# Optimization experiments

Hardware: AMD Instinct MI355X
Metric: run time of the kernel (lower is better)

## Reference

```python
import jax, jax.numpy as jnp
import numpy as np

N, E, H, G = 50000, 600000, 128, 512
PI = 3.141592653589793
EPS = 1e-5
NEG_SLOPE = 0.2


def _p(key, shape, scale):
    return jax.random.normal(key, shape, dtype=jnp.float32) * scale


def setup_inputs() -> dict:
    key = jax.random.key(0)
    ks = jax.random.split(key, 32)
    s = 1.0 / np.sqrt(H)
    inp = {
        "x": jax.random.normal(ks[0], (N, H), dtype=jnp.float32),
        "edge_index": jax.random.randint(ks[1], (2, E), 0, N, dtype=jnp.int32),
        "edge_attr": jax.random.normal(ks[2], (E, H), dtype=jnp.float32),
        "batch": jnp.sort(jax.random.randint(ks[3], (N,), 0, G, dtype=jnp.int32)),
    }
    # GATv2Conv layer 1 params
    inp.update(Wl1=_p(ks[4], (H, H), s), bl1=jnp.zeros((H,)), Wr1=_p(ks[5], (H, H), s), br1=jnp.zeros((H,)),
               We1=_p(ks[6], (H, H), s), att1=_p(ks[7], (H,), s), cb1=jnp.zeros((H,)))
    # GATv2Conv layer 2 params
    inp.update(Wl2=_p(ks[8], (H, H), s), bl2=jnp.zeros((H,)), Wr2=_p(ks[9], (H, H), s), br2=jnp.zeros((H,)),
               We2=_p(ks[10], (H, H), s), att2=_p(ks[11], (H,), s), cb2=jnp.zeros((H,)))
    # BatchNorm params
    inp.update(g1=jnp.ones((H,)), be1=jnp.zeros((H,)), g2=jnp.ones((H,)), be2=jnp.zeros((H,)))
    # AttentionalAggregation gate MLP (AggregationModuleTanh)
    inp.update(A1=_p(ks[12], (H, H), s), a1=jnp.zeros((H,)), A2=_p(ks[13], (H, H), s), a2=jnp.zeros((H,)))
    # final Linear
    inp.update(Wf=_p(ks[14], (H, H), s), bf=jnp.zeros((H,)))
    return inp


def gatv2(x, src, dst, eattr, Wl, bl, Wr, br, We, att, cb):
    n = x.shape[0]
    # add self loops, edge_attr fill_value='mean' (PyG default): per-dst mean of edge_attr
    deg = jax.ops.segment_sum(jnp.ones_like(dst, dtype=x.dtype), dst, num_segments=n)
    loop_attr = jax.ops.segment_sum(eattr, dst, num_segments=n) / jnp.maximum(deg, 1.0)[:, None]
    ar = jnp.arange(n, dtype=src.dtype)
    src2 = jnp.concatenate([src, ar])
    dst2 = jnp.concatenate([dst, ar])
    ea2 = jnp.concatenate([eattr, loop_attr], axis=0)
    xl = x @ Wl + bl  # source transform
    xr = x @ Wr + br  # target transform
    m = xl[src2] + xr[dst2] + ea2 @ We  # [E+N, H]
    m = jnp.where(m > 0, m, NEG_SLOPE * m)  # leaky_relu(0.2)
    e = m @ att  # [E+N]
    emax = jax.ops.segment_max(e, dst2, num_segments=n)
    ex = jnp.exp(e - emax[dst2])
    den = jax.ops.segment_sum(ex, dst2, num_segments=n)
    alpha = ex / den[dst2]
    out = jax.ops.segment_sum(alpha[:, None] * xl[src2], dst2, num_segments=n)
    return out + cb


def batchnorm(x, g, b):
    mu = jnp.mean(x, axis=0)
    var = jnp.var(x, axis=0)
    return (x - mu) * jax.lax.rsqrt(var + EPS) * g + b


def attn_pool(x, batch, A1, a1, A2, a2, n_graphs):
    gate = jnp.tanh(x @ A1 + a1) @ A2 + a2  # [N, H]
    gmax = jax.ops.segment_max(gate, batch, num_segments=n_graphs)
    ex = jnp.exp(gate - gmax[batch])
    den = jax.ops.segment_sum(ex, batch, num_segments=n_graphs)
    alpha = ex / jnp.maximum(den, 1e-16)[batch]
    return jax.ops.segment_sum(alpha * x, batch, num_segments=n_graphs)


def reference(x, edge_index, edge_attr, batch,
              Wl1, bl1, Wr1, br1, We1, att1, cb1,
              Wl2, bl2, Wr2, br2, We2, att2, cb2,
              g1, be1, g2, be2, A1, a1, A2, a2, Wf, bf):
    src, dst = edge_index[0], edge_index[1]
    h = gatv2(x, src, dst, edge_attr, Wl1, bl1, Wr1, br1, We1, att1, cb1)
    h = jnp.tanh(batchnorm(h, g1, be1))  # dropout = identity (eval)
    h = gatv2(h, src, dst, edge_attr, Wl2, bl2, Wr2, br2, We2, att2, cb2)
    h = jnp.tanh(batchnorm(h, g2, be2))
    pooled = attn_pool(h, batch, A1, a1, A2, a2, G)  # [G, H]
    out = jnp.tanh(pooled @ Wf + bf)
    axis = out * PI
    aperture = jnp.zeros_like(axis)
    return axis, aperture
```

## Files before the change

kernel.cpp:

```cpp
#include <hip/hip_runtime.h>
#include <hip/hip_bf16.h>
#include <math.h>

constexpr int NN = 50000;
constexpr int NE = 600000;
constexpr int HD = 128;
constexpr int NG = 512;
constexpr float EPSV = 1e-5f;
constexpr float PI_F = 3.14159265358979323846f;

static __device__ __forceinline__ float wave_reduce(float v) {
#pragma unroll
  for (int off = 32; off > 0; off >>= 1) v += __shfl_xor(v, off, 64);
  return v;
}

__global__ void deg_hist(const int* __restrict__ dst, int* __restrict__ deg) {
  int i = blockIdx.x * 256 + threadIdx.x;
  if (i < NE) atomicAdd(&deg[dst[i]], 1);
}

__global__ void scanA(const int* __restrict__ deg, int* __restrict__ part) {
  __shared__ int sh[256];
  int b = blockIdx.x, tid = threadIdx.x;
  int sum = 0;
  for (int k = tid; k < 1024; k += 256) {
    int idx = b * 1024 + k;
    if (idx < NN) sum += deg[idx];
  }
  sh[tid] = sum; __syncthreads();
  for (int s = 128; s; s >>= 1) { if (tid < s) sh[tid] += sh[tid + s]; __syncthreads(); }
  if (tid == 0) part[b] = sh[0];
}

__global__ void scanB(int* __restrict__ part, int nb) {
  if (threadIdx.x == 0) {
    int run = 0;
    for (int i = 0; i < nb; ++i) { int v = part[i]; part[i] = run; run += v; }
  }
}

__global__ void scanC(const int* __restrict__ deg, const int* __restrict__ part,
                      int* __restrict__ rowstart, int* __restrict__ cursor) {
  __shared__ int sh[256];
  int b = blockIdx.x, tid = threadIdx.x;
  int base = b * 1024 + tid * 4;
  int v[4];
#pragma unroll
  for (int k = 0; k < 4; ++k) v[k] = (base + k < NN) ? deg[base + k] : 0;
  int tot = v[0] + v[1] + v[2] + v[3];
  sh[tid] = tot; __syncthreads();
  for (int off = 1; off < 256; off <<= 1) {
    int x = (tid >= off) ? sh[tid - off] : 0;
    __syncthreads();
    sh[tid] += x;
    __syncthreads();
  }
  int excl = part[b] + sh[tid] - tot;
#pragma unroll
  for (int k = 0; k < 4; ++k) {
    if (base + k < NN) { rowstart[base + k] = excl; cursor[base + k] = excl; excl += v[k]; }
  }
}

__global__ void scatter_k(const int* __restrict__ src, const int* __restrict__ dst,
                          int* __restrict__ cursor, int* __restrict__ ceid, int* __restrict__ csrc) {
  int i = blockIdx.x * 256 + threadIdx.x;
  if (i < NE) {
    int d = dst[i];
    int pos = atomicAdd(&cursor[d], 1);
    ceid[pos] = i;
    csrc[pos] = src[i];
  }
}

__global__ void sloop_k(const float* __restrict__ eattr, const int* __restrict__ rowstart,
                        const int* __restrict__ deg, const int* __restrict__ ceid,
                        float* __restrict__ sloop) {
  int tid = threadIdx.x;
  int j = tid & 127, half = tid >> 7;
  int n = blockIdx.x * 2 + half;
  if (n >= NN) return;
  int st = rowstart[n], cnt = deg[n];
  float a = 0.f;
  for (int k = 0; k < cnt; ++k) {
    int e = ceid[st + k];
    a += eattr[(size_t)e * HD + j];
  }
  sloop[(size_t)n * HD + j] = a / (float)max(cnt, 1);
}

template <int DUAL, int ACT>
__global__ __launch_bounds__(256) void node_gemm(
    const float* __restrict__ in, const float* __restrict__ W1, const float* __restrict__ b1,
    const float* __restrict__ W2, const float* __restrict__ b2,
    float* __restrict__ o1, float* __restrict__ o2) {
  __shared__ float xs[32][HD];
  const int tid = threadIdx.x;
  const int j = tid & 127;
  const int half = tid >> 7;
  const int r0 = blockIdx.x * 32;
  for (int k = tid; k < 32 * HD / 4; k += 256) {
    int r = k >> 5, c4 = k & 31;
    float4 v = make_float4(0.f, 0.f, 0.f, 0.f);
    if (r0 + r < NN) v = ((const float4*)(in + (size_t)(r0 + r) * HD))[c4];
    *((float4*)&xs[r][c4 * 4]) = v;
  }
  __syncthreads();
  float acc1[16], acc2[16];
  const float bb1 = b1[j];
#pragma unroll
  for (int k = 0; k < 16; ++k) acc1[k] = bb1;
  if (DUAL) {
    const float bb2 = b2[j];
#pragma unroll
    for (int k = 0; k < 16; ++k) acc2[k] = bb2;
  }
#pragma unroll 4
  for (int i = 0; i < HD; i += 4) {
    const float w10 = W1[(i + 0) * HD + j], w11 = W1[(i + 1) * HD + j];
    const float w12 = W1[(i + 2) * HD + j], w13 = W1[(i + 3) * HD + j];
    float w20 = 0.f, w21 = 0.f, w22 = 0.f, w23 = 0.f;
    if (DUAL) {
      w20 = W2[(i + 0) * HD + j]; w21 = W2[(i + 1) * HD + j];
      w22 = W2[(i + 2) * HD + j]; w23 = W2[(i + 3) * HD + j];
    }
#pragma unroll
    for (int k = 0; k < 16; ++k) {
      const float4 a = *(const float4*)&xs[half * 16 + k][i];
      acc1[k] = fmaf(a.x, w10, fmaf(a.y, w11, fmaf(a.z, w12, fmaf(a.w, w13, acc1[k]))));
      if (DUAL)
        acc2[k] = fmaf(a.x, w20, fmaf(a.y, w21, fmaf(a.z, w22, fmaf(a.w, w23, acc2[k]))));
    }
  }
#pragma unroll
  for (int k = 0; k < 16; ++k) {
    int r = r0 + half * 16 + k;
    if (r < NN) {
      float v1 = acc1[k];
      if (ACT) v1 = tanhf(v1);
      o1[(size_t)r * HD + j] = v1;
      if (DUAL) o2[(size_t)r * HD + j] = acc2[k];
    }
  }
}

constexpr int ETOT = NE + NN;
constexpr int NTIL = (ETOT + 63) / 64;

static __device__ __forceinline__ void stage_ea(const float* __restrict__ eattr,
                                                const float* __restrict__ sloop,
                                                float* buf, int e0, int w, int lane) {
#pragma unroll
  for (int t = 0; t < 4; ++t) {
    const int rr = (w * 4 + t) * 2 + (lane >> 5);
    const int e = e0 + rr;
    const float* gp;
    if (e < NE) gp = eattr + (size_t)e * HD + (lane & 31) * 4;
    else if (e < ETOT) gp = sloop + (size_t)(e - NE) * HD + (lane & 31) * 4;
    else gp = eattr + (lane & 31) * 4;
    __builtin_amdgcn_global_load_lds(
        (const __attribute__((address_space(1))) void*)gp,
        (__attribute__((address_space(3))) void*)(buf + (w * 4 + t) * 256),
        16, 0, 0);
  }
}

__global__ __launch_bounds__(512, 2) void edge_scores(
    const float* __restrict__ eattr, const float* __restrict__ sloop,
    const int* __restrict__ src, const int* __restrict__ dst,
    const float* __restrict__ xl, const float* __restrict__ xr,
    const float* __restrict__ We, const float* __restrict__ att,
    float* __restrict__ ev) {
  __shared__ float We_s[HD * HD];
  __shared__ float ea_s[2][64 * HD];
  const int tid = threadIdx.x;
  const int tc = tid & 31;
  const int teg = tid >> 5;
  const int w = tid >> 6;
  const int lane = tid & 63;

  for (int k = tid; k < HD * HD / 4; k += 512)
    ((float4*)We_s)[k] = ((const float4*)We)[k];
  const float4 attv = ((const float4*)att)[tc];

  int it = blockIdx.x;
  int cur = 0;
  if (it < NTIL) stage_ea(eattr, sloop, ea_s[0], it * 64, w, lane);

  for (; it < NTIL; it += gridDim.x) {
    asm volatile("s_waitcnt vmcnt(0)" ::: "memory");
    __syncthreads();
    const int nxt = it + (int)gridDim.x;
    if (nxt < NTIL) stage_ea(eattr, sloop, ea_s[cur ^ 1], nxt * 64, w, lane);

    const float* ea = ea_s[cur];
    float acc[4][4];
#pragma unroll
    for (int m = 0; m < 4; ++m)
#pragma unroll
      for (int c = 0; c < 4; ++c) acc[m][c] = 0.f;

#pragma unroll 4
    for (int k0 = 0; k0 < HD; k0 += 4) {
      const float4 w0 = *(const float4*)&We_s[(k0 + 0) * HD + tc * 4];
      const float4 w1 = *(const float4*)&We_s[(k0 + 1) * HD + tc * 4];
      const float4 w2 = *(const float4*)&We_s[(k0 + 2) * HD + tc * 4];
      const float4 w3 = *(const float4*)&We_s[(k0 + 3) * HD + tc * 4];
#pragma unroll
      for (int m = 0; m < 4; ++m) {
        const float4 a = *(const float4*)&ea[(teg * 4 + m) * HD + k0];
        acc[m][0] = fmaf(a.x, w0.x, fmaf(a.y, w1.x, fmaf(a.z, w2.x, fmaf(a.w, w3.x, acc[m][0]))));
        acc[m][1] = fmaf(a.x, w0.y, fmaf(a.y, w1.y, fmaf(a.z, w2.y, fmaf(a.w, w3.y, acc[m][1]))));
        acc[m][2] = fmaf(a.x, w0.z, fmaf(a.y, w1.z, fmaf(a.z, w2.z, fmaf(a.w, w3.z, acc[m][2]))));
        acc[m][3] = fmaf(a.x, w0.w, fmaf(a.y, w1.w, fmaf(a.z, w2.w, fmaf(a.w, w3.w, acc[m][3]))));
      }
    }

    const int e0 = it * 64;
#pragma unroll
    for (int m = 0; m < 4; ++m) {
      const int e = e0 + teg * 4 + m;
      const bool valid = e < ETOT;
      int s_, d_;
      if (e < NE) { s_ = src[e]; d_ = dst[e]; }
      else if (valid) { s_ = d_ = e - NE; }
      else { s_ = d_ = 0; }
      const float4 xa = ((const float4*)(xl + (size_t)s_ * HD))[tc];
      const float4 xb = ((const float4*)(xr + (size_t)d_ * HD))[tc];
      float v0 = acc[m][0] + xa.x + xb.x; v0 = v0 > 0.f ? v0 : 0.2f * v0;
      float v1 = acc[m][1] + xa.y + xb.y; v1 = v1 > 0.f ? v1 : 0.2f * v1;
      float v2 = acc[m][2] + xa.z + xb.z; v2 = v2 > 0.f ? v2 : 0.2f * v2;
      float v3 = acc[m][3] + xa.w + xb.w; v3 = v3 > 0.f ? v3 : 0.2f * v3;
      float p = fmaf(v0, attv.x, fmaf(v1, attv.y, fmaf(v2, attv.z, v3 * attv.w)));
#pragma unroll
      for (int off = 1; off < 32; off <<= 1) p += __shfl_xor(p, off, 64);
      if (tc == 0 && valid) ev[e] = p;
    }
    cur ^= 1;
  }
}

__global__ void aggregate(const float* __restrict__ xl, const float* __restrict__ evals,
                          const int* __restrict__ rowstart, const int* __restrict__ deg,
                          const int* __restrict__ ceid, const int* __restrict__ csrc,
                          const float* __restrict__ cb, float* __restrict__ hout) {
  int tid = threadIdx.x;
  int j = tid & 127, half = tid >> 7;
  int n = blockIdx.x * 2 + half;
  if (n >= NN) return;
  int st = rowstart[n], cnt = deg[n];
  float m = evals[NE + n];
  float s = 1.f;
  float p = xl[(size_t)n * HD + j];
  for (int k = 0; k < cnt; ++k) {
    int e = ceid[st + k];
    int sc = csrc[st + k];
    float evv = evals[e];
    float x = xl[(size_t)sc * HD + j];
    float nm = fmaxf(m, evv);
    float c = __expf(m - nm);
    float w = __expf(evv - nm);
    s = s * c + w;
    p = p * c + w * x;
    m = nm;
  }
  hout[(size_t)n * HD + j] = p / s + cb[j];
}

__global__ void colstats(const float* __restrict__ h, float* __restrict__ cs, float* __restrict__ csq) {
  __shared__ float s1[256], s2[256];
  int tid = threadIdx.x;
  int j = tid & 127, half = tid >> 7;
  int rbeg = blockIdx.x * 256, rend = min(NN, rbeg + 256);
  float a = 0.f, b = 0.f;
  for (int r = rbeg + half; r < rend; r += 2) {
    float v = h[(size_t)r * HD + j];
    a += v; b += v * v;
  }
  s1[tid] = a; s2[tid] = b; __syncthreads();
  if (half == 0) {
    atomicAdd(&cs[j], s1[j] + s1[128 + j]);
    atomicAdd(&csq[j], s2[j] + s2[128 + j]);
  }
}

__global__ void bnfinal(const float* __restrict__ cs, const float* __restrict__ csq,
                        const float* __restrict__ g, const float* __restrict__ be,
                        float* __restrict__ scale, float* __restrict__ shift) {
  int j = threadIdx.x;
  float mu = cs[j] / (float)NN;
  float var = csq[j] / (float)NN - mu * mu;
  float sc = g[j] * rsqrtf(var + EPSV);
  scale[j] = sc;
  shift[j] = be[j] - mu * sc;
}

__global__ void bn_tanh(const float4* __restrict__ h, const float* __restrict__ scale,
                        const float* __restrict__ shift, float4* __restrict__ o) {
  const int n4 = NN * HD / 4;
  for (int i = blockIdx.x * blockDim.x + threadIdx.x; i < n4; i += gridDim.x * blockDim.x) {
    int c4 = i & 31;
    float4 v = h[i];
    float4 sc = ((const float4*)scale)[c4];
    float4 sh = ((const float4*)shift)[c4];
    float4 r;
    r.x = tanhf(fmaf(v.x, sc.x, sh.x));
    r.y = tanhf(fmaf(v.y, sc.y, sh.y));
    r.z = tanhf(fmaf(v.z, sc.z, sh.z));
    r.w = tanhf(fmaf(v.w, sc.w, sh.w));
    o[i] = r;
  }
}

__global__ void ranges_k(const int* __restrict__ batch, int* __restrict__ gstart, int* __restrict__ gend) {
  int i = blockIdx.x * 256 + threadIdx.x;
  if (i < NN) {
    int b = batch[i];
    atomicMin(&gstart[b], i);
    atomicMax(&gend[b], i + 1);
  }
}

__global__ void pool_k(const float* __restrict__ gate, const float* __restrict__ xin,
                       const int* __restrict__ gstart, const int* __restrict__ gend,
                       float* __restrict__ pooled) {
  const int g = blockIdx.x, j = threadIdx.x;
  const int st = gstart[g];
  if (st == 0x7f7f7f7f) { pooled[(size_t)g * HD + j] = 0.f; return; }
  const int en = gend[g];
  float m = -INFINITY, s = 0.f, p = 0.f;
  for (int n = st; n < en; ++n) {
    const float gv = gate[(size_t)n * HD + j];
    const float hv = xin[(size_t)n * HD + j];
    const float nm = fmaxf(m, gv);
    const float c = __expf(m - nm);
    const float w = __expf(gv - nm);
    s = s * c + w;
    p = p * c + w * hv;
    m = nm;
  }
  pooled[(size_t)g * HD + j] = p / fmaxf(s, 1e-16f);
}

__global__ void final_k(const float* __restrict__ pooled, const float* __restrict__ Wf,
                        const float* __restrict__ bf, float* __restrict__ out) {
  __shared__ float ps[HD];
  const int g = blockIdx.x, j = threadIdx.x;
  ps[j] = pooled[(size_t)g * HD + j];
  __syncthreads();
  float acc = bf[j];
#pragma unroll 8
  for (int i = 0; i < HD; ++i) acc = fmaf(ps[i], Wf[i * HD + j], acc);
  out[(size_t)g * HD + j] = tanhf(acc) * PI_F;
  out[(size_t)(NG + g) * HD + j] = 0.f;
}

extern "C" void kernel_launch(void* const* d_in, const int* in_sizes, int n_in,
                              void* d_out, int out_size, void* d_ws, size_t ws_size,
                              hipStream_t stream) {
  const float* x     = (const float*)d_in[0];
  const int*   eidx  = (const int*)d_in[1];
  const float* eattr = (const float*)d_in[2];
  const int*   batch = (const int*)d_in[3];
  const float *Wl1 = (const float*)d_in[4],  *bl1 = (const float*)d_in[5];
  const float *Wr1 = (const float*)d_in[6],  *br1 = (const float*)d_in[7];
  const float *We1 = (const float*)d_in[8],  *att1 = (const float*)d_in[9],  *cb1 = (const float*)d_in[10];
  const float *Wl2 = (const float*)d_in[11], *bl2 = (const float*)d_in[12];
  const float *Wr2 = (const float*)d_in[13], *br2 = (const float*)d_in[14];
  const float *We2 = (const float*)d_in[15], *att2 = (const float*)d_in[16], *cb2 = (const float*)d_in[17];
  const float *g1 = (const float*)d_in[18],  *be1 = (const float*)d_in[19];
  const float *g2 = (const float*)d_in[20],  *be2 = (const float*)d_in[21];
  const float *A1 = (const float*)d_in[22],  *a1 = (const float*)d_in[23];
  const float *A2 = (const float*)d_in[24],  *a2 = (const float*)d_in[25];
  const float *Wf = (const float*)d_in[26],  *bf = (const float*)d_in[27];
  const int* src = eidx;
  const int* dst = eidx + NE;

  float* ws = (float*)d_ws;
  const size_t NH = (size_t)NN * HD;
  float* sloopb = ws;
  float* xl     = ws + NH;
  float* xr     = ws + 2 * NH;
  float* hbuf   = ws + 3 * NH;
  float* hpr    = ws + 4 * NH;
  float* ev     = ws + 5 * NH;
  float* cs     = ev + (NE + NN);
  float* csq    = cs + HD;
  float* scale  = csq + HD;
  float* shift  = scale + HD;
  float* pooled = shift + HD;
  int* ideg     = (int*)(pooled + (size_t)NG * HD);
  int* rowstart = ideg + NN;
  int* cursor   = rowstart + NN;
  int* ceid     = cursor + NN;
  int* csrc     = ceid + NE;
  int* gstart   = csrc + NE;
  int* gend     = gstart + NG;
  int* part     = gend + NG;

  const int nbScan = (NN + 1023) / 1024;
  const int nbE = (NE + 255) / 256;
  const int nbN = (NN + 255) / 256;

  hipMemsetAsync(ideg, 0, NN * sizeof(int), stream);
  hipMemsetAsync(gstart, 0x7f, NG * sizeof(int), stream);
  hipMemsetAsync(gend, 0, NG * sizeof(int), stream);
  deg_hist<<<nbE, 256, 0, stream>>>(dst, ideg);
  scanA<<<nbScan, 256, 0, stream>>>(ideg, part);
  scanB<<<1, 64, 0, stream>>>(part, nbScan);
  scanC<<<nbScan, 256, 0, stream>>>(ideg, part, rowstart, cursor);
  scatter_k<<<nbE, 256, 0, stream>>>(src, dst, cursor, ceid, csrc);
  sloop_k<<<NN / 2, 256, 0, stream>>>(eattr, rowstart, ideg, ceid, sloopb);

  node_gemm<1, 0><<<(NN + 31) / 32, 256, 0, stream>>>(x, Wl1, bl1, Wr1, br1, xl, xr);
  edge_scores<<<256, 512, 0, stream>>>(eattr, sloopb, src, dst, xl, xr, We1, att1, ev);
  aggregate<<<NN / 2, 256, 0, stream>>>(xl, ev, rowstart, ideg, ceid, csrc, cb1, hbuf);
  hipMemsetAsync(cs, 0, 2 * HD * sizeof(float), stream);
  colstats<<<nbN, 256, 0, stream>>>(hbuf, cs, csq);
  bnfinal<<<1, 128, 0, stream>>>(cs, csq, g1, be1, scale, shift);
  bn_tanh<<<1024, 256, 0, stream>>>((const float4*)hbuf, scale, shift, (float4*)hpr);

  node_gemm<1, 0><<<(NN + 31) / 32, 256, 0, stream>>>(hpr, Wl2, bl2, Wr2, br2, xl, xr);
  edge_scores<<<256, 512, 0, stream>>>(eattr, sloopb, src, dst, xl, xr, We2, att2, ev);
  aggregate<<<NN / 2, 256, 0, stream>>>(xl, ev, rowstart, ideg, ceid, csrc, cb2, hbuf);
  hipMemsetAsync(cs, 0, 2 * HD * sizeof(float), stream);
  colstats<<<nbN, 256, 0, stream>>>(hbuf, cs, csq);
  bnfinal<<<1, 128, 0, stream>>>(cs, csq, g2, be2, scale, shift);
  bn_tanh<<<1024, 256, 0, stream>>>((const float4*)hbuf, scale, shift, (float4*)hpr);

  node_gemm<0, 1><<<(NN + 31) / 32, 256, 0, stream>>>(hpr, A1, a1, nullptr, nullptr, xr, nullptr);
  node_gemm<0, 0><<<(NN + 31) / 32, 256, 0, stream>>>(xr, A2, a2, nullptr, nullptr, xl, nullptr);
  ranges_k<<<nbN, 256, 0, stream>>>(batch, gstart, gend);
  pool_k<<<NG, 128, 0, stream>>>(xl, hpr, gstart, gend, pooled);
  final_k<<<NG, 128, 0, stream>>>(pooled, Wf, bf, (float*)d_out);
}
```

Measured before the change: 2.164 ms.

## Compute edge-attr projection with split-bf16 MFMA instead of FP32 FMA

```diff
diff --git a/kernel.cpp b/kernel.cpp
--- a/kernel.cpp
+++ b/kernel.cpp
@@ -9,11 +9,8 @@
 constexpr float EPSV = 1e-5f;
 constexpr float PI_F = 3.14159265358979323846f;
 
-static __device__ __forceinline__ float wave_reduce(float v) {
-#pragma unroll
-  for (int off = 32; off > 0; off >>= 1) v += __shfl_xor(v, off, 64);
-  return v;
-}
+typedef short s16x8 __attribute__((ext_vector_type(8)));
+typedef float f32x4 __attribute__((ext_vector_type(4)));
 
 __global__ void deg_hist(const int* __restrict__ dst, int* __restrict__ deg) {
   int i = blockIdx.x * 256 + threadIdx.x;
@@ -146,24 +143,15 @@
 }
 
 constexpr int ETOT = NE + NN;
-constexpr int NTIL = (ETOT + 63) / 64;
-
-static __device__ __forceinline__ void stage_ea(const float* __restrict__ eattr,
-                                                const float* __restrict__ sloop,
-                                                float* buf, int e0, int w, int lane) {
-#pragma unroll
-  for (int t = 0; t < 4; ++t) {
-    const int rr = (w * 4 + t) * 2 + (lane >> 5);
-    const int e = e0 + rr;
-    const float* gp;
-    if (e < NE) gp = eattr + (size_t)e * HD + (lane & 31) * 4;
-    else if (e < ETOT) gp = sloop + (size_t)(e - NE) * HD + (lane & 31) * 4;
-    else gp = eattr + (lane & 31) * 4;
-    __builtin_amdgcn_global_load_lds(
-        (const __attribute__((address_space(1))) void*)gp,
-        (__attribute__((address_space(3))) void*)(buf + (w * 4 + t) * 256),
-        16, 0, 0);
-  }
+constexpr int NTIL2 = (ETOT + 127) / 128;
+
+__device__ __forceinline__ void bf16split(float v, short& h, short& lo) {
+  unsigned u = __float_as_uint(v);
+  unsigned hu = (u + 0x7FFFu + ((u >> 16) & 1u)) & 0xFFFF0000u;
+  float lof = v - __uint_as_float(hu);
+  unsigned lu = __float_as_uint(lof);
+  h = (short)(hu >> 16);
+  lo = (short)((lu + 0x7FFFu + ((lu >> 16) & 1u)) >> 16);
 }
 
 __global__ __launch_bounds__(512, 2) void edge_scores(
@@ -172,72 +160,151 @@
     const float* __restrict__ xl, const float* __restrict__ xr,
     const float* __restrict__ We, const float* __restrict__ att,
     float* __restrict__ ev) {
-  __shared__ float We_s[HD * HD];
-  __shared__ float ea_s[2][64 * HD];
+  __shared__ unsigned short eh_s[128 * 128];
+  __shared__ unsigned short el_s[128 * 128];
+  __shared__ float zbuf[128 * 128];
   const int tid = threadIdx.x;
-  const int tc = tid & 31;
-  const int teg = tid >> 5;
+  const int l = tid & 63;
   const int w = tid >> 6;
-  const int lane = tid & 63;
-
-  for (int k = tid; k < HD * HD / 4; k += 512)
-    ((float4*)We_s)[k] = ((const float4*)We)[k];
-  const float4 attv = ((const float4*)att)[tc];
-
+  const int cbg = w & 3;
+  const int ebg = w >> 2;
+  const int l15 = l & 15;
+  const int l16 = l >> 4;
+
+  s16x8 bh[2][4], bl[2][4];
+#pragma unroll
+  for (int icb = 0; icb < 2; ++icb) {
+    const int c = cbg * 32 + icb * 16 + l15;
+#pragma unroll
+    for (int kk = 0; kk < 4; ++kk) {
+#pragma unroll
+      for (int j = 0; j < 8; ++j) {
+        const int k = kk * 32 + 8 * l16 + j;
+        short h_, lo_;
+        bf16split(We[k * HD + c], h_, lo_);
+        bh[icb][kk][j] = h_;
+        bl[icb][kk][j] = lo_;
+      }
+    }
+  }
+
+  const int se = tid >> 2;
+  const int kq = tid & 3;
+  const int half = l >> 5;
+  const int c4 = l & 31;
+  const float4 attv = ((const float4*)att)[c4];
+
+  float gl[32];
   int it = blockIdx.x;
-  int cur = 0;
-  if (it < NTIL) stage_ea(eattr, sloop, ea_s[0], it * 64, w, lane);
-
-  for (; it < NTIL; it += gridDim.x) {
-    asm volatile("s_waitcnt vmcnt(0)" ::: "memory");
+
+  if (it < NTIL2) {
+    const int e = it * 128 + se;
+    const float* rp = (e < NE) ? eattr + (size_t)e * HD
+                   : (e < ETOT ? sloop + (size_t)(e - NE) * HD : eattr);
+#pragma unroll
+    for (int i = 0; i < 8; ++i) *(float4*)&gl[4 * i] = ((const float4*)(rp + kq * 32))[i];
+#pragma unroll
+    for (int i = 0; i < 4; ++i) {
+      s16x8 vh, vl;
+#pragma unroll
+      for (int j = 0; j < 8; ++j) {
+        short h_, lo_;
+        bf16split(gl[8 * i + j], h_, lo_);
+        vh[j] = h_; vl[j] = lo_;
+      }
+      const int chunk = (kq * 4 + i) ^ (se & 7);
+      *(s16x8*)&eh_s[se * 128 + chunk * 8] = vh;
+      *(s16x8*)&el_s[se * 128 + chunk * 8] = vl;
+    }
+  }
+
+  for (; it < NTIL2; it += gridDim.x) {
+    const int nxt = it + (int)gridDim.x;
+    if (nxt < NTIL2) {
+      const int e = nxt * 128 + se;
+      const float* rp = (e < NE) ? eattr + (size_t)e * HD
+                     : (e < ETOT ? sloop + (size_t)(e - NE) * HD : eattr);
+#pragma unroll
+      for (int i = 0; i < 8; ++i) *(float4*)&gl[4 * i] = ((const float4*)(rp + kq * 32))[i];
+    }
     __syncthreads();
-    const int nxt = it + (int)gridDim.x;
-    if (nxt < NTIL) stage_ea(eattr, sloop, ea_s[cur ^ 1], nxt * 64, w, lane);
-
-    const float* ea = ea_s[cur];
-    float acc[4][4];
-#pragma unroll
-    for (int m = 0; m < 4; ++m)
-#pragma unroll
-      for (int c = 0; c < 4; ++c) acc[m][c] = 0.f;
-
-#pragma unroll 4
-    for (int k0 = 0; k0 < HD; k0 += 4) {
-      const float4 w0 = *(const float4*)&We_s[(k0 + 0) * HD + tc * 4];
-      const float4 w1 = *(const float4*)&We_s[(k0 + 1) * HD + tc * 4];
-      const float4 w2 = *(const float4*)&We_s[(k0 + 2) * HD + tc * 4];
-      const float4 w3 = *(const float4*)&We_s[(k0 + 3) * HD + tc * 4];
-#pragma unroll
-      for (int m = 0; m < 4; ++m) {
-        const float4 a = *(const float4*)&ea[(teg * 4 + m) * HD + k0];
-        acc[m][0] = fmaf(a.x, w0.x, fmaf(a.y, w1.x, fmaf(a.z, w2.x, fmaf(a.w, w3.x, acc[m][0]))));
-        acc[m][1] = fmaf(a.x, w0.y, fmaf(a.y, w1.y, fmaf(a.z, w2.y, fmaf(a.w, w3.y, acc[m][1]))));
-        acc[m][2] = fmaf(a.x, w0.z, fmaf(a.y, w1.z, fmaf(a.z, w2.z, fmaf(a.w, w3.z, acc[m][2]))));
-        acc[m][3] = fmaf(a.x, w0.w, fmaf(a.y, w1.w, fmaf(a.z, w2.w, fmaf(a.w, w3.w, acc[m][3]))));
+
+    f32x4 acc[4][2];
+#pragma unroll
+    for (int ie = 0; ie < 4; ++ie)
+#pragma unroll
+      for (int icb = 0; icb < 2; ++icb) acc[ie][icb] = (f32x4){0.f, 0.f, 0.f, 0.f};
+
+#pragma unroll
+    for (int kk = 0; kk < 4; ++kk) {
+      s16x8 Ah[4], Al[4];
+      const int chunk = ((kk * 4 + l16) ^ (l & 7)) * 8;
+#pragma unroll
+      for (int ie = 0; ie < 4; ++ie) {
+        const int eloc = ebg * 64 + ie * 16 + l15;
+        Ah[ie] = *(const s16x8*)&eh_s[eloc * 128 + chunk];
+        Al[ie] = *(const s16x8*)&el_s[eloc * 128 + chunk];
       }
-    }
-
-    const int e0 = it * 64;
-#pragma unroll
-    for (int m = 0; m < 4; ++m) {
-      const int e = e0 + teg * 4 + m;
+#pragma unroll
+      for (int ie = 0; ie < 4; ++ie) {
+#pragma unroll
+        for (int icb = 0; icb < 2; ++icb) {
+          acc[ie][icb] = __builtin_amdgcn_mfma_f32_16x16x32_bf16(Ah[ie], bh[icb][kk], acc[ie][icb], 0, 0, 0);
+          acc[ie][icb] = __builtin_amdgcn_mfma_f32_16x16x32_bf16(Al[ie], bh[icb][kk], acc[ie][icb], 0, 0, 0);
+          acc[ie][icb] = __builtin_amdgcn_mfma_f32_16x16x32_bf16(Ah[ie], bl[icb][kk], acc[ie][icb], 0, 0, 0);
+        }
+      }
+    }
+
+#pragma unroll
+    for (int ie = 0; ie < 4; ++ie)
+#pragma unroll
+      for (int icb = 0; icb < 2; ++icb)
+#pragma unroll
+        for (int r = 0; r < 4; ++r) {
+          const int eloc = ebg * 64 + ie * 16 + l16 * 4 + r;
+          const int c = cbg * 32 + icb * 16 + l15;
+          zbuf[eloc * 128 + (c ^ ((eloc & 7) << 2))] = acc[ie][icb][r];
+        }
+    __syncthreads();
+
+#pragma unroll
+    for (int ii = 0; ii < 8; ++ii) {
+      const int eloc = w * 16 + ii * 2 + half;
+      const int e = it * 128 + eloc;
       const bool valid = e < ETOT;
-      int s_, d_;
+      int s_ = 0, d_ = 0;
       if (e < NE) { s_ = src[e]; d_ = dst[e]; }
       else if (valid) { s_ = d_ = e - NE; }
-      else { s_ = d_ = 0; }
-      const float4 xa = ((const float4*)(xl + (size_t)s_ * HD))[tc];
-      const float4 xb = ((const float4*)(xr + (size_t)d_ * HD))[tc];
-      float v0 = acc[m][0] + xa.x + xb.x; v0 = v0 > 0.f ? v0 : 0.2f * v0;
-      float v1 = acc[m][1] + xa.y + xb.y; v1 = v1 > 0.f ? v1 : 0.2f * v1;
-      float v2 = acc[m][2] + xa.z + xb.z; v2 = v2 > 0.f ? v2 : 0.2f * v2;
-      float v3 = acc[m][3] + xa.w + xb.w; v3 = v3 > 0.f ? v3 : 0.2f * v3;
-      float p = fmaf(v0, attv.x, fmaf(v1, attv.y, fmaf(v2, attv.z, v3 * attv.w)));
+      const float4 zv = *(const float4*)&zbuf[eloc * 128 + ((c4 ^ (eloc & 7)) << 2)];
+      const float4 ga = ((const float4*)(xl + (size_t)s_ * HD))[c4];
+      const float4 gb = ((const float4*)(xr + (size_t)d_ * HD))[c4];
+      float m0 = zv.x + ga.x + gb.x; m0 = m0 > 0.f ? m0 : 0.2f * m0;
+      float m1 = zv.y + ga.y + gb.y; m1 = m1 > 0.f ? m1 : 0.2f * m1;
+      float m2 = zv.z + ga.z + gb.z; m2 = m2 > 0.f ? m2 : 0.2f * m2;
+      float m3 = zv.w + ga.w + gb.w; m3 = m3 > 0.f ? m3 : 0.2f * m3;
+      float p = fmaf(m0, attv.x, fmaf(m1, attv.y, fmaf(m2, attv.z, m3 * attv.w)));
 #pragma unroll
       for (int off = 1; off < 32; off <<= 1) p += __shfl_xor(p, off, 64);
-      if (tc == 0 && valid) ev[e] = p;
-    }
-    cur ^= 1;
+      if ((l & 31) == 0 && valid) ev[e] = p;
+    }
+    __syncthreads();
+
+    if (nxt < NTIL2) {
+#pragma unroll
+      for (int i = 0; i < 4; ++i) {
+        s16x8 vh, vl;
+#pragma unroll
+        for (int j = 0; j < 8; ++j) {
+          short h_, lo_;
+          bf16split(gl[8 * i + j], h_, lo_);
+          vh[j] = h_; vl[j] = lo_;
+        }
+        const int chunk = (kq * 4 + i) ^ (se & 7);
+        *(s16x8*)&eh_s[se * 128 + chunk * 8] = vh;
+        *(s16x8*)&el_s[se * 128 + chunk * 8] = vl;
+      }
+    }
   }
 }
 
```

Result: faster. 1.778 ms (-17.8%).
